# Optimization experiments

Hardware: AMD Instinct MI355X
Metric: run time of the kernel (lower is better)

The kernel has to match this reference:

```python
import jax, jax.numpy as jnp
import numpy as np

B, T, N, D = 8, 12, 512, 128
K = 16                      # number of pattern clusters
GEO_H, SEM_H, T_H = 4, 2, 2
HD = D // (GEO_H + SEM_H + T_H)      # 16
SCALE = HD ** -0.5
GD, SD, TD = GEO_H * HD, SEM_H * HD, T_H * HD  # 64, 32, 32


def setup_inputs() -> dict:
    key = jax.random.key(0)
    ks = jax.random.split(key, 24)
    w = lambda k, o, i: jax.random.normal(k, (o, i), jnp.float32) * 0.02
    return {
        'x': jax.random.normal(ks[0], (B, T, N, D), jnp.float32),
        'x_patterns': jax.random.normal(ks[1], (B, T, N, D, 1), jnp.float32),
        'pattern_keys': jax.random.normal(ks[2], (K, D, 1), jnp.float32),
        'dynamic_adj': jax.random.normal(ks[3], (B, N, N), jnp.float32) * 0.1,
        'geo_mask': jax.random.randint(ks[4], (N, N), 0, 2).astype(bool),
        'sem_mask': jax.random.randint(ks[5], (N, N), 0, 2).astype(bool),
        't_qw': w(ks[6], TD, D), 't_kw': w(ks[7], TD, D), 't_vw': w(ks[8], TD, D),
        'geo_qw': w(ks[9], GD, D), 'geo_kw': w(ks[10], GD, D), 'geo_vw': w(ks[11], GD, D),
        'sem_qw': w(ks[12], SD, D), 'sem_kw': w(ks[13], SD, D), 'sem_vw': w(ks[14], SD, D),
        'pat_qw': w(ks[15], GD, D), 'pat_qb': jax.random.normal(ks[16], (GD,), jnp.float32) * 0.02,
        'pat_kw': w(ks[17], GD, D), 'pat_kb': jax.random.normal(ks[18], (GD,), jnp.float32) * 0.02,
        'pat_vw': w(ks[19], GD, D), 'pat_vb': jax.random.normal(ks[20], (GD,), jnp.float32) * 0.02,
        'proj_w': w(ks[21], D, D), 'proj_b': jax.random.normal(ks[22], (D,), jnp.float32) * 0.02,
    }


def reference(x, x_patterns, pattern_keys, dynamic_adj, geo_mask, sem_mask,
              t_qw, t_kw, t_vw, geo_qw, geo_kw, geo_vw, sem_qw, sem_kw, sem_vw,
              pat_qw, pat_qb, pat_kw, pat_kb, pat_vw, pat_vb, proj_w, proj_b):
    Bc, Tc, Nc, Dc = x.shape
    proj3 = lambda z, w: jnp.einsum('btnd,ed->btne', z, w)  # 1x1 conv over channels

    # ---- temporal branch: attention over T per node ----
    def t_heads(z):  # (B,T,N,TD) -> (B,N,h,T,hd)
        return z.transpose(0, 2, 1, 3).reshape(Bc, Nc, Tc, T_H, HD).transpose(0, 1, 3, 2, 4)
    tq, tk, tv = t_heads(proj3(x, t_qw)), t_heads(proj3(x, t_kw)), t_heads(proj3(x, t_vw))
    t_attn = jax.nn.softmax(jnp.einsum('bnhqd,bnhkd->bnhqk', tq, tk) * SCALE, axis=-1)
    t_x = jnp.einsum('bnhqk,bnhkd->bnhqd', t_attn, tv)
    t_x = t_x.transpose(0, 1, 3, 2, 4).reshape(Bc, Nc, Tc, TD).transpose(0, 2, 1, 3)  # (B,T,N,TD)

    # ---- geo branch: pattern attention augments geo_k ----
    geo_q, geo_k, geo_v = proj3(x, geo_qw), proj3(x, geo_kw), proj3(x, geo_vw)
    pq = x_patterns[..., 0] @ pat_qw.T + pat_qb          # (B,T,N,GD)
    pk = pattern_keys[..., 0] @ pat_kw.T + pat_kb        # (K,GD)
    pv = pattern_keys[..., 0] @ pat_vw.T + pat_vb        # (K,GD)
    p_attn = jax.nn.softmax(jnp.einsum('btne,ke->btnk', pq, pk) * SCALE, axis=-1)
    geo_k = geo_k + jnp.einsum('btnk,ke->btne', p_attn, pv)

    def s_heads(z, h):  # (B,T,N,h*hd) -> (B,T,h,N,hd)
        return z.reshape(Bc, Tc, Nc, h, HD).transpose(0, 1, 3, 2, 4)
    gq, gk, gv = s_heads(geo_q, GEO_H), s_heads(geo_k, GEO_H), s_heads(geo_v, GEO_H)
    g_attn = jnp.einsum('bthqd,bthkd->bthqk', gq, gk) * SCALE
    g_attn = g_attn + dynamic_adj[:, None, None]         # dynamic bias
    g_attn = jnp.where(geo_mask, -jnp.inf, g_attn)
    g_attn = jax.nn.softmax(g_attn, axis=-1)
    geo_x = jnp.einsum('bthqk,bthkd->bthqd', g_attn, gv)
    geo_x = geo_x.transpose(0, 1, 3, 2, 4).reshape(Bc, Tc, Nc, GD)

    # ---- semantic branch ----
    sq = s_heads(proj3(x, sem_qw), SEM_H)
    sk = s_heads(proj3(x, sem_kw), SEM_H)
    sv = s_heads(proj3(x, sem_vw), SEM_H)
    s_attn = jnp.einsum('bthqd,bthkd->bthqk', sq, sk) * SCALE
    s_attn = jnp.where(sem_mask, -jnp.inf, s_attn)
    s_attn = jax.nn.softmax(s_attn, axis=-1)
    sem_x = jnp.einsum('bthqk,bthkd->bthqd', s_attn, sv)
    sem_x = sem_x.transpose(0, 1, 3, 2, 4).reshape(Bc, Tc, Nc, SD)

    out = jnp.concatenate([t_x, geo_x, sem_x], axis=-1) @ proj_w.T + proj_b
    return out
```

## Files before the change

### kernel.cpp

```cpp
#include <hip/hip_runtime.h>
#include <hip/hip_bf16.h>

using bf16 = __hip_bfloat16;
typedef __attribute__((ext_vector_type(8))) short short8;
typedef __attribute__((ext_vector_type(4))) float f32x4;
typedef __attribute__((ext_vector_type(4))) unsigned int u32x4;

#define Bc 8
#define Tc 12
#define Nc 512
#define Dc 128
#define T_Hc 2
#define GEO_Hc 4
#define SEM_Hc 2
#define HDc 16
#define SCALEc 0.25f

constexpr size_t TSZ = (size_t)Bc * Nc * T_Hc * Tc * HDc;
constexpr size_t GSZ = (size_t)Bc * Tc * GEO_Hc * Nc * HDc;
constexpr size_t SSZ = (size_t)Bc * Tc * SEM_Hc * Nc * HDc;
constexpr size_t CSZ = (size_t)Bc * Tc * Nc * Dc;
constexpr size_t H_TQ = 0;
constexpr size_t H_TK = H_TQ + TSZ;
constexpr size_t H_TV = H_TK + TSZ;
constexpr size_t H_GQ = H_TV + TSZ;
constexpr size_t H_GK = H_GQ + GSZ;
constexpr size_t H_GV = H_GK + GSZ;
constexpr size_t H_SQ = H_GV + GSZ;
constexpr size_t H_SK = H_SQ + SSZ;
constexpr size_t H_SV = H_SK + SSZ;
constexpr size_t H_CC = H_SV + SSZ;
constexpr size_t H_END = H_CC + CSZ;
constexpr size_t F_PK = (H_END + 1) / 2;
constexpr size_t F_PV = F_PK + 1024;
constexpr size_t F_FLAG = F_PV + 1024;
constexpr size_t H_W2X = 2 * (F_FLAG + 64);
constexpr size_t H_W2O = H_W2X + 384 * 256;
constexpr size_t H_BG = H_TQ;
constexpr size_t H_BS = H_TQ + 2097152;

__device__ __forceinline__ float b2f(bf16 v) { return __bfloat162float(v); }
__device__ __forceinline__ bf16 f2b(float v) { return __float2bfloat16(v); }
__device__ __forceinline__ short f2bs(float v) {
    bf16 b = __float2bfloat16(v);
    return *reinterpret_cast<short*>(&b);
}
__device__ __forceinline__ float bs2f(short s) {
    union { unsigned u; float f; } x;
    x.u = ((unsigned)(unsigned short)s) << 16;
    return x.f;
}
__device__ __forceinline__ unsigned packbf(float a, float b) {
    unsigned ua = (unsigned)(unsigned short)f2bs(a);
    unsigned ub = (unsigned)(unsigned short)f2bs(b);
    return ua | (ub << 16);
}

__global__ __launch_bounds__(256) void k_prep(
    const float* __restrict__ pattern_keys, const float* __restrict__ pat_kw,
    const float* __restrict__ pat_kb, const float* __restrict__ pat_vw,
    const float* __restrict__ pat_vb, float* __restrict__ fws) {
    int idx = blockIdx.x * 256 + threadIdx.x;
    int which = idx >> 10;
    int r = idx & 1023;
    int k = r >> 6, e = r & 63;
    const float4* w = (const float4*)((which ? pat_vw : pat_kw) + (size_t)e * 128);
    const float4* pk = (const float4*)(pattern_keys + (size_t)k * 128);
    float acc = which ? pat_vb[e] : pat_kb[e];
#pragma unroll
    for (int j = 0; j < 32; ++j) {
        float4 a = pk[j], b = w[j];
        acc = fmaf(a.x, b.x, acc); acc = fmaf(a.y, b.y, acc);
        acc = fmaf(a.z, b.z, acc); acc = fmaf(a.w, b.w, acc);
    }
    fws[(which ? F_PV : F_PK) + (size_t)k * 64 + e] = acc;
}

__global__ __launch_bounds__(256) void k_maskdet(
    const unsigned char* __restrict__ mask, float* __restrict__ fws) {
    __shared__ int s_u8, s_odd4;
    int tid = threadIdx.x;
    if (tid == 0) { s_u8 = 0; s_odd4 = 0; }
    __syncthreads();
    int u8 = 0, odd4 = 0;
    for (int i = tid * 16; i < tid * 16 + 16; ++i) {
        unsigned char v = mask[i];
        if (v && (i & 3)) u8 = 1;
        if (v && ((i & 7) == 4)) odd4 = 1;
    }
    if (u8) atomicOr(&s_u8, 1);
    if (odd4) atomicOr(&s_odd4, 1);
    __syncthreads();
    if (tid == 0) fws[F_FLAG] = s_u8 ? 0.f : (s_odd4 ? 1.f : 2.f);
}

__device__ __forceinline__ const float* wrow(
    int gc, const float* tq, const float* tk, const float* tv,
    const float* gq, const float* gk, const float* gv,
    const float* sq, const float* sk, const float* sv) {
    if (gc < 32) return tq + (size_t)gc * 128;
    if (gc < 64) return tk + (size_t)(gc - 32) * 128;
    if (gc < 96) return tv + (size_t)(gc - 64) * 128;
    if (gc < 160) return gq + (size_t)(gc - 96) * 128;
    if (gc < 224) return gk + (size_t)(gc - 160) * 128;
    if (gc < 288) return gv + (size_t)(gc - 224) * 128;
    if (gc < 320) return sq + (size_t)(gc - 288) * 128;
    if (gc < 352) return sk + (size_t)(gc - 320) * 128;
    return sv + (size_t)(gc - 352) * 128;
}

__global__ __launch_bounds__(256) void k_wcvt(
    const float* __restrict__ t_qw, const float* __restrict__ t_kw,
    const float* __restrict__ t_vw, const float* __restrict__ geo_qw,
    const float* __restrict__ geo_kw, const float* __restrict__ geo_vw,
    const float* __restrict__ sem_qw, const float* __restrict__ sem_kw,
    const float* __restrict__ sem_vw, const float* __restrict__ proj_w,
    bf16* __restrict__ hb) {
    int gid = blockIdx.x * 256 + threadIdx.x;
    if (gid < 49152) {
        int row = gid >> 7, k = gid & 127;
        const float* src = wrow(row, t_qw, t_kw, t_vw, geo_qw, geo_kw, geo_vw,
                                sem_qw, sem_kw, sem_vw);
        float v = src[k];
        if ((row >= 96 && row < 160) || (row >= 288 && row < 320)) v *= SCALEc;
        bf16 bv = f2b(v);
        hb[H_W2X + (size_t)row * 256 + 2 * k] = bv;
        hb[H_W2X + (size_t)row * 256 + 2 * k + 1] = bv;
    } else {
        int g = gid - 49152;
        hb[H_W2O + g] = f2b(proj_w[g]);
    }
}

__global__ __launch_bounds__(256) void k_bias(
    const float* __restrict__ dyn, const unsigned char* __restrict__ gm,
    const unsigned char* __restrict__ sm, const float* __restrict__ fws,
    bf16* __restrict__ hb) {
    int bid = blockIdx.x;
    int tid = threadIdx.x;
    int mode = (int)fws[F_FLAG];
    if (bid < 8192) {
        int b = bid & 7;
        int inner = bid >> 3;
        size_t rem = (size_t)inner * 256 + tid;
        size_t gid = (size_t)b * 262144 + rem;
        int mv = (mode == 0) ? (int)gm[rem]
               : (mode == 1) ? ((const int*)gm)[rem]
                             : ((const int*)gm)[2 * rem];
        hb[H_BG + gid] = f2b(mv ? -1e30f : dyn[gid]);
    } else {
        size_t sid = (size_t)(bid - 8192) * 256 + tid;
        int mv = (mode == 0) ? (int)sm[sid]
               : (mode == 1) ? ((const int*)sm)[sid]
                             : ((const int*)sm)[2 * sid];
        hb[H_BS + sid] = f2b(mv ? -1e30f : 0.f);
    }
}

__global__ __launch_bounds__(256, 2) void k_projx(
    const float* __restrict__ x, bf16* __restrict__ hb) {
    __shared__ short xs[128 * 256];

    int tid = threadIdx.x;
    int m0 = blockIdx.x * 128;
    int b = m0 / (Tc * Nc);
    int rr = m0 - b * Tc * Nc;
    int t = rr >> 9;
    int n0 = rr & 511;

    for (int u = tid; u < 4096; u += 256) {
        int row = u >> 5, g = u & 31;
        float4 v = *(const float4*)(x + (size_t)(m0 + row) * 128 + g * 4);
        short8 s;
        short h0 = f2bs(v.x); s[0] = h0; s[1] = f2bs(v.x - bs2f(h0));
        short h1 = f2bs(v.y); s[2] = h1; s[3] = f2bs(v.y - bs2f(h1));
        short h2 = f2bs(v.z); s[4] = h2; s[5] = f2bs(v.z - bs2f(h2));
        short h3 = f2bs(v.w); s[6] = h3; s[7] = f2bs(v.w - bs2f(h3));
        *(short8*)&xs[row * 256 + ((g ^ (row & 7)) << 3)] = s;
    }
    __syncthreads();

    int w = tid >> 6;
    int lane = tid & 63;
    int l15 = lane & 15;
    int quad = lane >> 4;
    const bf16* w2 = hb + H_W2X;

    for (int nc = 0; nc < 6; ++nc) {
        f32x4 acc[2][4];
#pragma unroll
        for (int i = 0; i < 2; ++i)
#pragma unroll
            for (int j = 0; j < 4; ++j) acc[i][j] = (f32x4){0.f, 0.f, 0.f, 0.f};

#pragma unroll
        for (int ks = 0; ks < 8; ++ks) {
            int r0 = w * 32 + l15;
            int r1 = r0 + 16;
            short8 a0 = *(const short8*)&xs[r0 * 256 + (((ks * 4 + quad) ^ (r0 & 7)) << 3)];
            short8 a1 = *(const short8*)&xs[r1 * 256 + (((ks * 4 + quad) ^ (r1 & 7)) << 3)];
#pragma unroll
            for (int nj = 0; nj < 4; ++nj) {
                short8 bfr = *(const short8*)(w2 + (size_t)(nc * 64 + nj * 16 + l15) * 256
                                              + ks * 32 + quad * 8);
                acc[0][nj] = __builtin_amdgcn_mfma_f32_16x16x32_bf16(a0, bfr, acc[0][nj], 0, 0, 0);
                acc[1][nj] = __builtin_amdgcn_mfma_f32_16x16x32_bf16(a1, bfr, acc[1][nj], 0, 0, 0);
            }
        }
#pragma unroll
        for (int nj = 0; nj < 4; ++nj) {
            int gc = nc * 64 + nj * 16 + l15;
            int tile16 = nc * 4 + nj;
            int d = gc & 15;
#pragma unroll
            for (int i = 0; i < 2; ++i) {
                int nrow0 = n0 + w * 32 + i * 16 + quad * 4;
#pragma unroll
                for (int r = 0; r < 4; ++r) {
                    int n = nrow0 + r;
                    float v = acc[i][nj][r];
                    size_t idx;
                    if (tile16 < 6) {
                        int which = gc >> 5, hh = (gc >> 4) & 1;
                        size_t base = which == 0 ? H_TQ : which == 1 ? H_TK : H_TV;
                        idx = base + ((size_t)(b * Nc + n) * T_Hc + hh) * (Tc * HDc)
                              + t * HDc + d;
                    } else if (tile16 < 18) {
                        int r2 = gc - 96;
                        int which = r2 >> 6, hh = (r2 >> 4) & 3;
                        size_t base = which == 0 ? H_GQ : which == 1 ? H_GK : H_GV;
                        size_t sl = (((size_t)b * Tc + t) * GEO_Hc + hh) * (Nc * HDc);
                        idx = base + sl + (which == 2 ? ((size_t)d * Nc + n)
                                                      : ((size_t)n * HDc + d));
                    } else {
                        int r2 = gc - 288;
                        int which = r2 >> 5, hh = (r2 >> 4) & 1;
                        size_t base = which == 0 ? H_SQ : which == 1 ? H_SK : H_SV;
                        size_t sl = (((size_t)b * Tc + t) * SEM_Hc + hh) * (Nc * HDc);
                        idx = base + sl + (which == 2 ? ((size_t)d * Nc + n)
                                                      : ((size_t)n * HDc + d));
                    }
                    hb[idx] = f2b(v);
                }
            }
        }
    }
}

__global__ __launch_bounds__(256, 2) void k_projp(
    const float* __restrict__ xp, const float* __restrict__ pat_qw,
    const float* __restrict__ pat_qb, const float* __restrict__ fws,
    bf16* __restrict__ hb) {
    __shared__ float xs[64 * 132];
    __shared__ float wsh[64 * 68];
    __shared__ float pks[1024], pvs[1024], pqbs[64];

    int tid = threadIdx.x;
    int tok0 = blockIdx.x * 64;
    int ty = tid >> 4, tx = tid & 15;

    for (int u = tid; u < 2048; u += 256) {
        int row = u >> 5, f4 = u & 31;
        *(float4*)&xs[row * 132 + f4 * 4] =
            *(const float4*)(xp + (size_t)(tok0 + row) * 128 + f4 * 4);
    }
    for (int u = tid; u < 1024; u += 256) {
        pks[u] = fws[F_PK + u];
        pvs[u] = fws[F_PV + u];
    }
    if (tid < 64) pqbs[tid] = pat_qb[tid];

    float acc[4][4] = {};
    for (int kh = 0; kh < 2; ++kh) {
        __syncthreads();
        for (int u = tid; u < 1024; u += 256) {
            int row = u >> 4, f4 = u & 15;
            *(float4*)&wsh[row * 68 + f4 * 4] =
                *(const float4*)(pat_qw + (size_t)row * 128 + kh * 64 + f4 * 4);
        }
        __syncthreads();
#pragma unroll 4
        for (int kk = 0; kk < 64; kk += 4) {
            float4 a[4], b[4];
#pragma unroll
            for (int i = 0; i < 4; ++i)
                a[i] = *(const float4*)&xs[(ty + 16 * i) * 132 + kh * 64 + kk];
#pragma unroll
            for (int j = 0; j < 4; ++j)
                b[j] = *(const float4*)&wsh[(tx + 16 * j) * 68 + kk];
#pragma unroll
            for (int i = 0; i < 4; ++i)
#pragma unroll
                for (int j = 0; j < 4; ++j) {
                    acc[i][j] = fmaf(a[i].x, b[j].x, acc[i][j]);
                    acc[i][j] = fmaf(a[i].y, b[j].y, acc[i][j]);
                    acc[i][j] = fmaf(a[i].z, b[j].z, acc[i][j]);
                    acc[i][j] = fmaf(a[i].w, b[j].w, acc[i][j]);
                }
        }
    }
    __syncthreads();
    float* pqs = xs;
    float* plogs = wsh;
#pragma unroll
    for (int i = 0; i < 4; ++i)
#pragma unroll
        for (int j = 0; j < 4; ++j)
            pqs[(ty + 16 * i) * 68 + tx + 16 * j] = acc[i][j] + pqbs[tx + 16 * j];
    __syncthreads();
    {
        int tok = tid >> 2, k4 = (tid & 3) * 4;
        for (int k = k4; k < k4 + 4; ++k) {
            float s = 0.f;
#pragma unroll 16
            for (int e = 0; e < 64; ++e)
                s = fmaf(pqs[tok * 68 + e], pks[k * 64 + e], s);
            plogs[tok * 17 + k] = s * SCALEc;
        }
    }
    __syncthreads();
    {
        int tok = tid >> 2, q = tid & 3;
        float mx = -1e30f;
        for (int k = 0; k < 16; ++k) mx = fmaxf(mx, plogs[tok * 17 + k]);
        float p[16], sum = 0.f;
        for (int k = 0; k < 16; ++k) {
            p[k] = __expf(plogs[tok * 17 + k] - mx);
            sum += p[k];
        }
        float inv = 1.f / sum;
        int token = tok0 + tok;
        int b = token / (Tc * Nc);
        int rr = token - b * Tc * Nc;
        int t = rr >> 9;
        int n = rr & 511;
        for (int cc = 0; cc < 16; ++cc) {
            int c = q * 16 + cc;
            float v = 0.f;
            for (int k = 0; k < 16; ++k) v = fmaf(p[k], pvs[k * 64 + c], v);
            v *= inv;
            size_t idx = H_GK + (((size_t)b * Tc + t) * GEO_Hc + (c >> 4)) * (Nc * HDc)
                         + n * HDc + (c & 15);
            hb[idx] = f2b(b2f(hb[idx]) + v);
        }
    }
}

__global__ __launch_bounds__(64) void k_tattn(bf16* __restrict__ hb) {
    int blk = blockIdx.x;
    int h = blk & 1;
    int bn = blk >> 1;
    int b = bn >> 9;
    int n = bn & 511;
    size_t base = ((size_t)(b * Nc + n) * T_Hc + h) * (Tc * HDc);

    __shared__ float q[192], kk[192], v[192], s[144];
    int tid = threadIdx.x;
    for (int u = tid; u < 192; u += 64) {
        q[u] = b2f(hb[H_TQ + base + u]);
        kk[u] = b2f(hb[H_TK + base + u]);
        v[u] = b2f(hb[H_TV + base + u]);
    }
    __syncthreads();
    for (int idx = tid; idx < 144; idx += 64) {
        int qi = idx / 12, ki = idx - qi * 12;
        float acc = 0.f;
#pragma unroll
        for (int d = 0; d < 16; ++d) acc = fmaf(q[qi * 16 + d], kk[ki * 16 + d], acc);
        s[idx] = acc * SCALEc;
    }
    __syncthreads();
    if (tid < 12) {
        float mx = -1e30f;
        for (int ki = 0; ki < 12; ++ki) mx = fmaxf(mx, s[tid * 12 + ki]);
        float sum = 0.f;
        for (int ki = 0; ki < 12; ++ki) {
            float p = __expf(s[tid * 12 + ki] - mx);
            s[tid * 12 + ki] = p;
            sum += p;
        }
        float inv = 1.f / sum;
        for (int ki = 0; ki < 12; ++ki) s[tid * 12 + ki] *= inv;
    }
    __syncthreads();
    for (int idx = tid; idx < 192; idx += 64) {
        int qi = idx >> 4, d = idx & 15;
        float acc = 0.f;
#pragma unroll
        for (int ki = 0; ki < 12; ++ki) acc = fmaf(s[qi * 12 + ki], v[ki * 16 + d], acc);
        hb[H_CC + (((size_t)b * Tc + qi) * Nc + n) * Dc + h * HDc + d] = f2b(acc);
    }
}

__global__ __launch_bounds__(256, 8) void k_attn2m(bf16* __restrict__ hb) {
    __shared__ short vt[16 * 512];

    int bid = blockIdx.x;
    int b = bid & 7;
    int rem = bid >> 3;
    int m3 = rem % 3;
    int d3 = rem / 3;

    int H, coff, lb;
    size_t QO, KO, VO, bstride;
    const bf16* bias0;
    if (m3 == 2) {
        H = SEM_Hc; coff = 96; QO = H_SQ; KO = H_SK; VO = H_SV;
        bias0 = hb + H_BS; bstride = 0; lb = d3;
    } else {
        H = GEO_Hc; coff = 32; QO = H_GQ; KO = H_GK; VO = H_GV;
        bias0 = hb + H_BG; bstride = (size_t)Nc * Nc; lb = 2 * d3 + m3;
    }
    int part = lb & 7;
    int th = lb >> 3;
    int h = th % H;
    int t = th / H;

    size_t bth = (((size_t)b * Tc + t) * H + h) * (size_t)(Nc * HDc);
    const bf16* Qp = hb + QO + bth;
    const bf16* Kp = hb + KO + bth;
    const bf16* Vg = hb + VO + bth;
    const bf16* bp = bias0 + (size_t)b * bstride;

    int tid = threadIdx.x;

    for (int u = tid; u < 1024; u += 256) {
        int d = u >> 6, gg = u & 63;
        *(short8*)&vt[d * 512 + ((gg ^ (d & 7)) << 3)] =
            *(const short8*)(Vg + (size_t)d * 512 + gg * 8);
    }
    __syncthreads();

    int lane = tid & 63;
    int w = tid >> 6;
    int l15 = lane & 15;
    int quad = lane >> 4;
    int sw = l15 & 7;
    int srcA = l15 + ((lane & 16) << 1);
    int srcB = srcA + 16;
    bool hi = lane >= 32;

    union U8 { u32x4 u; short8 s; };

    int q0 = part * 64 + w * 16;
    int qg = q0 + l15;
    short8 bq = {0, 0, 0, 0, 0, 0, 0, 0};
    if (quad < 2) bq = *(const short8*)(Qp + (size_t)qg * 16 + quad * 8);

    float l_i = 0.f;
    f32x4 O = {0.f, 0.f, 0.f, 0.f};

    for (int ch = 0; ch < 4; ++ch) {
        int kabs0 = ch * 128;
        f32x4 S[8];
#pragma unroll
        for (int kt = 0; kt < 8; ++kt) {
            int kabs = kabs0 + kt * 16;
            short4 bb = *(const short4*)(bp + (size_t)qg * 512 + kabs + quad * 4);
            f32x4 c;
            c[0] = bs2f(bb.x); c[1] = bs2f(bb.y);
            c[2] = bs2f(bb.z); c[3] = bs2f(bb.w);
            short8 ak = {0, 0, 0, 0, 0, 0, 0, 0};
            if (quad < 2)
                ak = *(const short8*)(Kp + (size_t)(kabs + l15) * 16 + quad * 8);
            S[kt] = __builtin_amdgcn_mfma_f32_16x16x32_bf16(ak, bq, c, 0, 0, 0);
        }
        unsigned pk2[8][2];
        float psum = 0.f;
#pragma unroll
        for (int kt = 0; kt < 8; ++kt) {
            float p0 = __expf(S[kt][0]);
            float p1 = __expf(S[kt][1]);
            float p2 = __expf(S[kt][2]);
            float p3 = __expf(S[kt][3]);
            psum += (p0 + p1) + (p2 + p3);
            pk2[kt][0] = packbf(p0, p1);
            pk2[kt][1] = packbf(p2, p3);
        }
        psum += __shfl_xor(psum, 16);
        psum += __shfl_xor(psum, 32);
        l_i += psum;
#pragma unroll
        for (int kw = 0; kw < 4; ++kw) {
            unsigned eA0 = __shfl(pk2[2 * kw][0], srcA);
            unsigned eA1 = __shfl(pk2[2 * kw][1], srcA);
            unsigned oA0 = __shfl(pk2[2 * kw + 1][0], srcA);
            unsigned oA1 = __shfl(pk2[2 * kw + 1][1], srcA);
            unsigned eB0 = __shfl(pk2[2 * kw][0], srcB);
            unsigned eB1 = __shfl(pk2[2 * kw][1], srcB);
            unsigned oB0 = __shfl(pk2[2 * kw + 1][0], srcB);
            unsigned oB1 = __shfl(pk2[2 * kw + 1][1], srcB);
            U8 ap;
            ap.u = (u32x4){hi ? oA0 : eA0, hi ? oA1 : eA1,
                           hi ? oB0 : eB0, hi ? oB1 : eB1};
            short8 bv = *(const short8*)&vt[l15 * 512
                             + (((ch * 16 + kw * 4 + quad) ^ sw) << 3)];
            O = __builtin_amdgcn_mfma_f32_16x16x32_bf16(ap.s, bv, O, 0, 0, 0);
        }
    }
    float li0 = __shfl(l_i, (quad << 2) | 0);
    float li1 = __shfl(l_i, (quad << 2) | 1);
    float li2 = __shfl(l_i, (quad << 2) | 2);
    float li3 = __shfl(l_i, (quad << 2) | 3);
    size_t obase = H_CC + (((size_t)b * Tc + t) * Nc + q0) * Dc + coff + h * HDc + l15;
    hb[obase + (size_t)(quad * 4 + 0) * Dc] = f2b(O[0] / li0);
    hb[obase + (size_t)(quad * 4 + 1) * Dc] = f2b(O[1] / li1);
    hb[obase + (size_t)(quad * 4 + 2) * Dc] = f2b(O[2] / li2);
    hb[obase + (size_t)(quad * 4 + 3) * Dc] = f2b(O[3] / li3);
}

__global__ __launch_bounds__(256, 3) void k_outm(
    const bf16* __restrict__ hb, const float* __restrict__ proj_b,
    float* __restrict__ out) {
    __shared__ short cs[128 * 128];
    __shared__ float pbs[128];

    int tid = threadIdx.x;
    int m0 = blockIdx.x * 128;

    for (int u = tid; u < 2048; u += 256) {
        int row = u >> 4, g = u & 15;
        *(short8*)&cs[row * 128 + ((g ^ (row & 7)) << 3)] =
            *(const short8*)(hb + H_CC + (size_t)(m0 + row) * 128 + g * 8);
    }
    if (tid < 128) pbs[tid] = proj_b[tid];
    __syncthreads();

    int w = tid >> 6;
    int lane = tid & 63;
    int l15 = lane & 15;
    int quad = lane >> 4;
    const bf16* w2o = hb + H_W2O;

    f32x4 acc[2][8];
#pragma unroll
    for (int i = 0; i < 2; ++i)
#pragma unroll
        for (int j = 0; j < 8; ++j) acc[i][j] = (f32x4){0.f, 0.f, 0.f, 0.f};

#pragma unroll
    for (int ks = 0; ks < 4; ++ks) {
        int r0 = w * 32 + l15;
        int r1 = r0 + 16;
        short8 a0 = *(const short8*)&cs[r0 * 128 + (((ks * 4 + quad) ^ (r0 & 7)) << 3)];
        short8 a1 = *(const short8*)&cs[r1 * 128 + (((ks * 4 + quad) ^ (r1 & 7)) << 3)];
#pragma unroll
        for (int nj = 0; nj < 8; ++nj) {
            short8 bfr = *(const short8*)(w2o + (size_t)(nj * 16 + l15) * 128
                                          + ks * 32 + quad * 8);
            acc[0][nj] = __builtin_amdgcn_mfma_f32_16x16x32_bf16(a0, bfr, acc[0][nj], 0, 0, 0);
            acc[1][nj] = __builtin_amdgcn_mfma_f32_16x16x32_bf16(a1, bfr, acc[1][nj], 0, 0, 0);
        }
    }
#pragma unroll
    for (int i = 0; i < 2; ++i) {
#pragma unroll
        for (int nj = 0; nj < 8; ++nj) {
            int ch = nj * 16 + l15;
            float bias = pbs[ch];
#pragma unroll
            for (int r = 0; r < 4; ++r) {
                int token = m0 + w * 32 + i * 16 + quad * 4 + r;
                out[(size_t)token * 128 + ch] = acc[i][nj][r] + bias;
            }
        }
    }
}

extern "C" void kernel_launch(void* const* d_in, const int* in_sizes, int n_in,
                              void* d_out, int out_size, void* d_ws, size_t ws_size,
                              hipStream_t stream) {
    const float* x = (const float*)d_in[0];
    const float* xp = (const float*)d_in[1];
    const float* pattern_keys = (const float*)d_in[2];
    const float* dyn = (const float*)d_in[3];
    const void* geo_mask = d_in[4];
    const void* sem_mask = d_in[5];
    const float* t_qw = (const float*)d_in[6];
    const float* t_kw = (const float*)d_in[7];
    const float* t_vw = (const float*)d_in[8];
    const float* geo_qw = (const float*)d_in[9];
    const float* geo_kw = (const float*)d_in[10];
    const float* geo_vw = (const float*)d_in[11];
    const float* sem_qw = (const float*)d_in[12];
    const float* sem_kw = (const float*)d_in[13];
    const float* sem_vw = (const float*)d_in[14];
    const float* pat_qw = (const float*)d_in[15];
    const float* pat_qb = (const float*)d_in[16];
    const float* pat_kw = (const float*)d_in[17];
    const float* pat_kb = (const float*)d_in[18];
    const float* pat_vw = (const float*)d_in[19];
    const float* pat_vb = (const float*)d_in[20];
    const float* proj_w = (const float*)d_in[21];
    const float* proj_b = (const float*)d_in[22];

    bf16* hb = (bf16*)d_ws;
    float* fws = (float*)d_ws;

    k_prep<<<8, 256, 0, stream>>>(pattern_keys, pat_kw, pat_kb, pat_vw, pat_vb, fws);
    k_maskdet<<<1, 256, 0, stream>>>((const unsigned char*)geo_mask, fws);
    k_wcvt<<<256, 256, 0, stream>>>(t_qw, t_kw, t_vw, geo_qw, geo_kw, geo_vw,
                                    sem_qw, sem_kw, sem_vw, proj_w, hb);
    k_projx<<<384, 256, 0, stream>>>(x, hb);
    k_projp<<<768, 256, 0, stream>>>(xp, pat_qw, pat_qb, fws, hb);
    k_tattn<<<Bc * Nc * T_Hc, 64, 0, stream>>>(hb);
    k_bias<<<9216, 256, 0, stream>>>(dyn, (const unsigned char*)geo_mask,
                                     (const unsigned char*)sem_mask, fws, hb);
    k_attn2m<<<Bc * Tc * (GEO_Hc + SEM_Hc) * 8, 256, 0, stream>>>(hb);
    k_outm<<<384, 256, 0, stream>>>(hb, proj_b, (float*)d_out);
}
```

Baseline: 352.6 us.

## Merge prep kernels, fold log2e into scales, use hardware exp2/rcp in attention

Merges the three small setup kernels (pattern key/value projection, mask format detection, weight conversion) into one launch to cut launch overhead. Folds log2(e) into the query weight scale and the bias/mask values so the masked spatial attention can use the raw v_exp_f32 exp2 instruction instead of __expf, and replaces the final division with v_rcp_f32. Raises wave priority around the PV MFMA loop. Hardware exp and rcp give slightly lower accuracy. Folding log2e into the weights and bias also changes the exponent base for any other kernel that reads those scaled q weights.

```diff
diff --git a/kernel.cpp b/kernel.cpp
--- a/kernel.cpp
+++ b/kernel.cpp
@@ -15,6 +15,7 @@
 #define SEM_Hc 2
 #define HDc 16
 #define SCALEc 0.25f
+#define LOG2E 1.4426950408889634f
 
 constexpr size_t TSZ = (size_t)Bc * Nc * T_Hc * Tc * HDc;
 constexpr size_t GSZ = (size_t)Bc * Tc * GEO_Hc * Nc * HDc;
@@ -55,43 +56,15 @@
     unsigned ub = (unsigned)(unsigned short)f2bs(b);
     return ua | (ub << 16);
 }
-
-__global__ __launch_bounds__(256) void k_prep(
-    const float* __restrict__ pattern_keys, const float* __restrict__ pat_kw,
-    const float* __restrict__ pat_kb, const float* __restrict__ pat_vw,
-    const float* __restrict__ pat_vb, float* __restrict__ fws) {
-    int idx = blockIdx.x * 256 + threadIdx.x;
-    int which = idx >> 10;
-    int r = idx & 1023;
-    int k = r >> 6, e = r & 63;
-    const float4* w = (const float4*)((which ? pat_vw : pat_kw) + (size_t)e * 128);
-    const float4* pk = (const float4*)(pattern_keys + (size_t)k * 128);
-    float acc = which ? pat_vb[e] : pat_kb[e];
-#pragma unroll
-    for (int j = 0; j < 32; ++j) {
-        float4 a = pk[j], b = w[j];
-        acc = fmaf(a.x, b.x, acc); acc = fmaf(a.y, b.y, acc);
-        acc = fmaf(a.z, b.z, acc); acc = fmaf(a.w, b.w, acc);
-    }
-    fws[(which ? F_PV : F_PK) + (size_t)k * 64 + e] = acc;
-}
-
-__global__ __launch_bounds__(256) void k_maskdet(
-    const unsigned char* __restrict__ mask, float* __restrict__ fws) {
-    __shared__ int s_u8, s_odd4;
-    int tid = threadIdx.x;
-    if (tid == 0) { s_u8 = 0; s_odd4 = 0; }
-    __syncthreads();
-    int u8 = 0, odd4 = 0;
-    for (int i = tid * 16; i < tid * 16 + 16; ++i) {
-        unsigned char v = mask[i];
-        if (v && (i & 3)) u8 = 1;
-        if (v && ((i & 7) == 4)) odd4 = 1;
-    }
-    if (u8) atomicOr(&s_u8, 1);
-    if (odd4) atomicOr(&s_odd4, 1);
-    __syncthreads();
-    if (tid == 0) fws[F_FLAG] = s_u8 ? 0.f : (s_odd4 ? 1.f : 2.f);
+__device__ __forceinline__ float exp2hw(float x) {
+    float r;
+    asm("v_exp_f32 %0, %1" : "=v"(r) : "v"(x));
+    return r;
+}
+__device__ __forceinline__ float rcphw(float x) {
+    float r;
+    asm("v_rcp_f32 %0, %1" : "=v"(r) : "v"(x));
+    return r;
 }
 
 __device__ __forceinline__ const float* wrow(
@@ -109,26 +82,62 @@
     return sv + (size_t)(gc - 352) * 128;
 }
 
-__global__ __launch_bounds__(256) void k_wcvt(
+__global__ __launch_bounds__(256) void k_prepw(
     const float* __restrict__ t_qw, const float* __restrict__ t_kw,
     const float* __restrict__ t_vw, const float* __restrict__ geo_qw,
     const float* __restrict__ geo_kw, const float* __restrict__ geo_vw,
     const float* __restrict__ sem_qw, const float* __restrict__ sem_kw,
     const float* __restrict__ sem_vw, const float* __restrict__ proj_w,
-    bf16* __restrict__ hb) {
-    int gid = blockIdx.x * 256 + threadIdx.x;
-    if (gid < 49152) {
-        int row = gid >> 7, k = gid & 127;
-        const float* src = wrow(row, t_qw, t_kw, t_vw, geo_qw, geo_kw, geo_vw,
-                                sem_qw, sem_kw, sem_vw);
-        float v = src[k];
-        if ((row >= 96 && row < 160) || (row >= 288 && row < 320)) v *= SCALEc;
-        bf16 bv = f2b(v);
-        hb[H_W2X + (size_t)row * 256 + 2 * k] = bv;
-        hb[H_W2X + (size_t)row * 256 + 2 * k + 1] = bv;
+    const float* __restrict__ pattern_keys, const float* __restrict__ pat_kw,
+    const float* __restrict__ pat_kb, const float* __restrict__ pat_vw,
+    const float* __restrict__ pat_vb, const unsigned char* __restrict__ mask,
+    bf16* __restrict__ hb, float* __restrict__ fws) {
+    if (blockIdx.x < 256) {
+        int gid = blockIdx.x * 256 + threadIdx.x;
+        if (gid < 49152) {
+            int row = gid >> 7, k = gid & 127;
+            const float* src = wrow(row, t_qw, t_kw, t_vw, geo_qw, geo_kw,
+                                    geo_vw, sem_qw, sem_kw, sem_vw);
+            float v = src[k];
+            if ((row >= 96 && row < 160) || (row >= 288 && row < 320))
+                v *= SCALEc * LOG2E;
+            bf16 bv = f2b(v);
+            hb[H_W2X + (size_t)row * 256 + 2 * k] = bv;
+            hb[H_W2X + (size_t)row * 256 + 2 * k + 1] = bv;
+        } else {
+            int g = gid - 49152;
+            hb[H_W2O + g] = f2b(proj_w[g]);
+        }
+    } else if (blockIdx.x < 264) {
+        int idx = (blockIdx.x - 256) * 256 + threadIdx.x;
+        int which = idx >> 10;
+        int r = idx & 1023;
+        int k = r >> 6, e = r & 63;
+        const float4* w = (const float4*)((which ? pat_vw : pat_kw) + (size_t)e * 128);
+        const float4* pk = (const float4*)(pattern_keys + (size_t)k * 128);
+        float acc = which ? pat_vb[e] : pat_kb[e];
+#pragma unroll
+        for (int j = 0; j < 32; ++j) {
+            float4 a = pk[j], b = w[j];
+            acc = fmaf(a.x, b.x, acc); acc = fmaf(a.y, b.y, acc);
+            acc = fmaf(a.z, b.z, acc); acc = fmaf(a.w, b.w, acc);
+        }
+        fws[(which ? F_PV : F_PK) + (size_t)k * 64 + e] = acc;
     } else {
-        int g = gid - 49152;
-        hb[H_W2O + g] = f2b(proj_w[g]);
+        __shared__ int s_u8, s_odd4;
+        int tid = threadIdx.x;
+        if (tid == 0) { s_u8 = 0; s_odd4 = 0; }
+        __syncthreads();
+        int u8 = 0, odd4 = 0;
+        for (int i = tid * 16; i < tid * 16 + 16; ++i) {
+            unsigned char v = mask[i];
+            if (v && (i & 3)) u8 = 1;
+            if (v && ((i & 7) == 4)) odd4 = 1;
+        }
+        if (u8) atomicOr(&s_u8, 1);
+        if (odd4) atomicOr(&s_odd4, 1);
+        __syncthreads();
+        if (tid == 0) fws[F_FLAG] = s_u8 ? 0.f : (s_odd4 ? 1.f : 2.f);
     }
 }
 
@@ -147,13 +156,13 @@
         int mv = (mode == 0) ? (int)gm[rem]
                : (mode == 1) ? ((const int*)gm)[rem]
                              : ((const int*)gm)[2 * rem];
-        hb[H_BG + gid] = f2b(mv ? -1e30f : dyn[gid]);
+        hb[H_BG + gid] = f2b(mv ? -1.44e30f : dyn[gid] * LOG2E);
     } else {
         size_t sid = (size_t)(bid - 8192) * 256 + tid;
         int mv = (mode == 0) ? (int)sm[sid]
                : (mode == 1) ? ((const int*)sm)[sid]
                              : ((const int*)sm)[2 * sid];
-        hb[H_BS + sid] = f2b(mv ? -1e30f : 0.f);
+        hb[H_BS + sid] = f2b(mv ? -1.44e30f : 0.f);
     }
 }
 
@@ -469,10 +478,10 @@
         float psum = 0.f;
 #pragma unroll
         for (int kt = 0; kt < 8; ++kt) {
-            float p0 = __expf(S[kt][0]);
-            float p1 = __expf(S[kt][1]);
-            float p2 = __expf(S[kt][2]);
-            float p3 = __expf(S[kt][3]);
+            float p0 = exp2hw(S[kt][0]);
+            float p1 = exp2hw(S[kt][1]);
+            float p2 = exp2hw(S[kt][2]);
+            float p3 = exp2hw(S[kt][3]);
             psum += (p0 + p1) + (p2 + p3);
             pk2[kt][0] = packbf(p0, p1);
             pk2[kt][1] = packbf(p2, p3);
@@ -480,6 +489,7 @@
         psum += __shfl_xor(psum, 16);
         psum += __shfl_xor(psum, 32);
         l_i += psum;
+        __builtin_amdgcn_s_setprio(1);
 #pragma unroll
         for (int kw = 0; kw < 4; ++kw) {
             unsigned eA0 = __shfl(pk2[2 * kw][0], srcA);
@@ -497,16 +507,17 @@
                              + (((ch * 16 + kw * 4 + quad) ^ sw) << 3)];
             O = __builtin_amdgcn_mfma_f32_16x16x32_bf16(ap.s, bv, O, 0, 0, 0);
         }
+        __builtin_amdgcn_s_setprio(0);
     }
     float li0 = __shfl(l_i, (quad << 2) | 0);
     float li1 = __shfl(l_i, (quad << 2) | 1);
     float li2 = __shfl(l_i, (quad << 2) | 2);
     float li3 = __shfl(l_i, (quad << 2) | 3);
     size_t obase = H_CC + (((size_t)b * Tc + t) * Nc + q0) * Dc + coff + h * HDc + l15;
-    hb[obase + (size_t)(quad * 4 + 0) * Dc] = f2b(O[0] / li0);
-    hb[obase + (size_t)(quad * 4 + 1) * Dc] = f2b(O[1] / li1);
-    hb[obase + (size_t)(quad * 4 + 2) * Dc] = f2b(O[2] / li2);
-    hb[obase + (size_t)(quad * 4 + 3) * Dc] = f2b(O[3] / li3);
+    hb[obase + (size_t)(quad * 4 + 0) * Dc] = f2b(O[0] * rcphw(li0));
+    hb[obase + (size_t)(quad * 4 + 1) * Dc] = f2b(O[1] * rcphw(li1));
+    hb[obase + (size_t)(quad * 4 + 2) * Dc] = f2b(O[2] * rcphw(li2));
+    hb[obase + (size_t)(quad * 4 + 3) * Dc] = f2b(O[3] * rcphw(li3));
 }
 
 __global__ __launch_bounds__(256, 3) void k_outm(
@@ -597,10 +608,11 @@
     bf16* hb = (bf16*)d_ws;
     float* fws = (float*)d_ws;
 
-    k_prep<<<8, 256, 0, stream>>>(pattern_keys, pat_kw, pat_kb, pat_vw, pat_vb, fws);
-    k_maskdet<<<1, 256, 0, stream>>>((const unsigned char*)geo_mask, fws);
-    k_wcvt<<<256, 256, 0, stream>>>(t_qw, t_kw, t_vw, geo_qw, geo_kw, geo_vw,
-                                    sem_qw, sem_kw, sem_vw, proj_w, hb);
+    k_prepw<<<265, 256, 0, stream>>>(t_qw, t_kw, t_vw, geo_qw, geo_kw, geo_vw,
+                                     sem_qw, sem_kw, sem_vw, proj_w,
+                                     pattern_keys, pat_kw, pat_kb, pat_vw,
+                                     pat_vb, (const unsigned char*)geo_mask,
+                                     hb, fws);
     k_projx<<<384, 256, 0, stream>>>(x, hb);
     k_projp<<<768, 256, 0, stream>>>(xp, pat_qw, pat_qb, fws, hb);
     k_tattn<<<Bc * Nc * T_Hc, 64, 0, stream>>>(hb);
```

New measurement: 338.4 us. 1.04x faster.
